# Performance work log

Measured on AMD Instinct MI355X. Metric: run time of the kernel, lower is better.

The kernel has to match this reference:

```python
import jax, jax.numpy as jnp
import numpy as np

N_NODES = 20000
N_EDGES = 80000
D = 128       # in_dim_node == in_dim_edge == hidden dims
ITERS = 15    # mp_iterations
EPS = 1e-5    # torch LayerNorm default eps


def _mlp(h, W0, b0, W1, b1, W2, b2, gamma, beta):
    """Linear-ReLU-Linear-ReLU-Linear-LayerNorm (hidden_layers=2)."""
    h = jax.nn.relu(h @ W0 + b0)
    h = jax.nn.relu(h @ W1 + b1)
    h = h @ W2 + b2
    mu = jnp.mean(h, axis=-1, keepdims=True)
    var = jnp.var(h, axis=-1, keepdims=True)
    return gamma * (h - mu) * jax.lax.rsqrt(var + EPS) + beta


def setup_inputs() -> dict:
    key = jax.random.key(0)
    ks = iter(jax.random.split(key, 32))

    def lin(fi, fo):
        bnd = 1.0 / np.sqrt(fi)
        W = jax.random.uniform(next(ks), (ITERS, fi, fo), minval=-bnd, maxval=bnd, dtype=jnp.float32)
        b = jax.random.uniform(next(ks), (ITERS, fo), minval=-bnd, maxval=bnd, dtype=jnp.float32)
        return W, b

    x = jax.random.normal(next(ks), (N_NODES, D), dtype=jnp.float32)
    edge_attr = jax.random.normal(next(ks), (N_EDGES, D), dtype=jnp.float32)
    edge_index = jax.random.randint(next(ks), (2, N_EDGES), 0, N_NODES)

    eW0, eB0 = lin(3 * D, D)   # edge MLP input = cat(src, dest, edge) = 384
    eW1, eB1 = lin(D, D)
    eW2, eB2 = lin(D, D)
    nW0, nB0 = lin(2 * D, D)   # node MLP input = cat(x, agg) = 256
    nW1, nB1 = lin(D, D)
    nW2, nB2 = lin(D, D)
    ones = jnp.ones((ITERS, D), jnp.float32)
    zeros = jnp.zeros((ITERS, D), jnp.float32)

    return dict(x=x, edge_attr=edge_attr,
                eW0=eW0, eB0=eB0, eW1=eW1, eB1=eB1, eW2=eW2, eB2=eB2, eG=ones, eBeta=zeros,
                nW0=nW0, nB0=nB0, nW1=nW1, nB1=nB1, nW2=nW2, nB2=nB2, nG=ones, nBeta=zeros,
                edge_index=edge_index)


def reference(x, edge_attr, eW0, eB0, eW1, eB1, eW2, eB2, eG, eBeta,
              nW0, nB0, nW1, nB1, nW2, nB2, nG, nBeta, edge_index):
    row, col = edge_index[0], edge_index[1]
    n = x.shape[0]
    params = (eW0, eB0, eW1, eB1, eW2, eB2, eG, eBeta,
              nW0, nB0, nW1, nB1, nW2, nB2, nG, nBeta)

    def step(carry, p):
        xc, ec = carry
        (ew0, eb0, ew1, eb1, ew2, eb2, eg, ebt,
         nw0, nb0, nw1, nb1, nw2, nb2, ng, nbt) = p
        # EdgeProcessor: gather + MLP, then FullResidualConnection (add previous)
        e_in = jnp.concatenate([xc[row], xc[col], ec], axis=-1)        # [E, 3D]
        ec = _mlp(e_in, ew0, eb0, ew1, eb1, ew2, eb2, eg, ebt) + ec
        # NodeProcessor: scatter_sum over destination nodes + MLP + residual
        agg = jax.ops.segment_sum(ec, col, num_segments=n)             # [N, D]
        n_in = jnp.concatenate([xc, agg], axis=-1)                     # [N, 2D]
        xc = _mlp(n_in, nw0, nb0, nw1, nb1, nw2, nb2, ng, nbt) + xc
        return (xc, ec), None

    (x, edge_attr), _ = jax.lax.scan(step, (x, edge_attr), params)
    return x, edge_attr
```

## Files before the change

### kernel.cpp

```cpp
#include <hip/hip_runtime.h>
#include <hip/hip_bf16.h>

typedef __hip_bfloat16 bf16;
typedef __attribute__((ext_vector_type(8))) short short8;
typedef __attribute__((ext_vector_type(4))) float f32x4;

#define NN 20000
#define NE 80000
#define DD 128
#define NITER 15
#define HSTRIDE 136

__device__ inline void gload16(const void* g, void* l) {
  __builtin_amdgcn_global_load_lds(
      (const __attribute__((address_space(1))) void*)g,
      (__attribute__((address_space(3))) void*)l, 16, 0, 0);
}

__device__ inline float bfbits2f(unsigned int hi16) {
  union { unsigned int u; float f; } c; c.u = hi16; return c.f;
}

__device__ inline float readin(const void* p, int i, int fl) {
  return fl ? (float)((const bf16*)p)[i] : ((const float*)p)[i];
}

__global__ void detzero_kernel(const unsigned short* __restrict__ x,
                               int* __restrict__ counts, int* __restrict__ flag) {
  const int bid = blockIdx.x, t = threadIdx.x;
  if (bid < 79) {
    int i = bid * 256 + t;
    if (i < NN) counts[i] = 0;
    return;
  }
  __shared__ int cs[256], ct[256];
  int sane = 0, tot = 0;
  for (int i = 2 * t; i < 16384; i += 512) {
    unsigned short v = x[i];
    int e = (v >> 7) & 0xFF;
    tot++;
    if (v == 0 || (e >= 80 && e <= 170)) sane++;
  }
  cs[t] = sane; ct[t] = tot;
  __syncthreads();
  for (int o = 128; o > 0; o >>= 1) {
    if (t < o) { cs[t] += cs[t + o]; ct[t] += ct[t + o]; }
    __syncthreads();
  }
  if (t == 0) *flag = (cs[0] * 10 > ct[0] * 7) ? 1 : 0;
}

#define CX  (NN * DD)
#define CE  (NE * DD)
#define CW0 (NITER * 384 * DD)
#define CW1 (NITER * 128 * DD)
#define CNW0 (NITER * 256 * DD)
#define CB  (NITER * DD)
#define BX0 CX
#define BX1 (BX0 + CE)
#define BX7 (BX1 + CW0 + CW1 + CW1 + CNW0 + CW1 + CW1)
#define BX8 (BX7 + 10 * CB)

struct CvtP {
  const void *x, *e;
  const void* w[6];
  bf16 *xb, *eb;
  bf16* wt[6];
  const void* bs[10];
  float* bd[10];
  const int* flag;
};

__global__ void convert_all(CvtP P) {
  const int fl = *P.flag;
  const int gstride = gridDim.x * 256;
  for (int i = blockIdx.x * 256 + threadIdx.x; i < BX8; i += gstride) {
    if (i < BX0) {
      P.xb[i] = (bf16)readin(P.x, i, fl);
    } else if (i < BX1) {
      P.eb[i - BX0] = (bf16)readin(P.e, i - BX0, fl);
    } else if (i < BX7) {
      int j = i - BX1, w;
      if (j < CW0) { w = 0; }
      else if ((j -= CW0) < CW1) { w = 1; }
      else if ((j -= CW1) < CW1) { w = 2; }
      else if ((j -= CW1) < CNW0) { w = 3; }
      else if ((j -= CNW0) < CW1) { w = 4; }
      else { j -= CW1; w = 5; }
      const int K = (w == 0) ? 384 : (w == 3) ? 256 : 128;
      float v = readin(P.w[w], j, fl);
      int it = j / (K * DD);
      int rem = j - it * K * DD;
      int k = rem >> 7, n = rem & 127;
      P.wt[w][(size_t)it * K * DD + (size_t)n * K + k] = (bf16)v;
    } else {
      int j = i - BX7;
      int b = j / CB, r = j - b * CB;
      P.bd[b][r] = readin(P.bs[b], r, fl);
    }
  }
}

template<int K0, int AMODE>
__global__ __launch_bounds__(256, 4) void fused_mlp(
    const bf16* S0b,
    const bf16* S1b,
    const int*  __restrict__ eidx,
    const bf16* __restrict__ W0t, const bf16* __restrict__ W1t,
    const bf16* __restrict__ W2t,
    const float* __restrict__ b0, const float* __restrict__ b1,
    const float* __restrict__ b2,
    const float* __restrict__ gamma, const float* __restrict__ beta,
    bf16* st, int M)
{
  constexpr int NS1 = K0 / 32;
  __shared__ __align__(16) bf16 Bls[2][128 * 32];
  __shared__ __align__(16) bf16 Hls[64 * HSTRIDE];

  const int tid  = threadIdx.x;
  const int lane = tid & 63;
  const int wv   = tid >> 6;
  const int l15  = lane & 15, quad = lane >> 4;
  const int m0   = blockIdx.x * 64;
  const int scol = tid >> 2;
  const int sk8  = (tid & 3) * 8;

  const int rowm = min(m0 + wv * 16 + l15, M - 1);
  int ir = 0, ic = 0;
  if (AMODE == 1) { ir = eidx[rowm]; ic = eidx[NE + rowm]; }

  auto dmaW = [&](const bf16* W, int K, int kk, int buf) {
    gload16(W + (size_t)scol * K + kk + sk8,        &Bls[buf][scol * 32 + sk8]);
    gload16(W + (size_t)(scol + 64) * K + kk + sk8, &Bls[buf][(scol + 64) * 32 + sk8]);
  };
  auto gatherA = [&](int kk, short8* a) {
    const int ks = (kk & 127) + quad * 8;
    const bf16* base;
    if (AMODE == 1) {
      const int seg = kk >> 7;
      base = (seg == 0) ? S0b + (size_t)ir * DD
           : (seg == 1) ? S0b + (size_t)ic * DD
                        : S1b + (size_t)rowm * DD;
    } else {
      base = (kk >> 7) ? S1b + (size_t)rowm * DD
                       : S0b + (size_t)rowm * DD;
    }
    *a = *(const short8*)(base + ks);
  };

  f32x4 acc[8];
  auto zacc = [&]() {
#pragma unroll
    for (int j = 0; j < 8; j++) acc[j] = (f32x4){0.f, 0.f, 0.f, 0.f};
  };
  auto slabMfmaA = [&](short8 a, int buf) {
    short8 bfr[8];
#pragma unroll
    for (int ni = 0; ni < 8; ni++)
      bfr[ni] = *(const short8*)&Bls[buf][(ni * 16 + l15) * 32 + quad * 8];
#pragma unroll
    for (int ni = 0; ni < 8; ni++)
      acc[ni] = __builtin_amdgcn_mfma_f32_16x16x32_bf16(a, bfr[ni], acc[ni], 0, 0, 0);
  };
  auto slabMfmaH = [&](int kk, int buf) {
    short8 a = *(const short8*)&Hls[(wv * 16 + l15) * HSTRIDE + kk + quad * 8];
    short8 bfr[8];
#pragma unroll
    for (int ni = 0; ni < 8; ni++)
      bfr[ni] = *(const short8*)&Bls[buf][(ni * 16 + l15) * 32 + quad * 8];
#pragma unroll
    for (int ni = 0; ni < 8; ni++)
      acc[ni] = __builtin_amdgcn_mfma_f32_16x16x32_bf16(a, bfr[ni], acc[ni], 0, 0, 0);
  };
  auto writeH = [&](const float* bias) {
    float bv[8];
#pragma unroll
    for (int ni = 0; ni < 8; ni++) bv[ni] = bias[ni * 16 + l15];
#pragma unroll
    for (int r = 0; r < 4; r++) {
      const int row = wv * 16 + quad * 4 + r;
#pragma unroll
      for (int ni = 0; ni < 8; ni++)
        Hls[row * HSTRIDE + ni * 16 + l15] = (bf16)fmaxf(acc[ni][r] + bv[ni], 0.f);
    }
  };

  zacc();
  short8 aCur, aNxt;
  dmaW(W0t, K0, 0, 0);
  gatherA(0, &aCur);
  __syncthreads();
#pragma unroll
  for (int s = 0; s < NS1; s++) {
    if (s + 1 < NS1) {
      dmaW(W0t, K0, (s + 1) * 32, (s + 1) & 1);
      gatherA((s + 1) * 32, &aNxt);
    } else {
      dmaW(W1t, 128, 0, NS1 & 1);
    }
    slabMfmaA(aCur, s & 1);
    __syncthreads();
    aCur = aNxt;
  }
  writeH(b0);
  __syncthreads();

  zacc();
#pragma unroll
  for (int s = 0; s < 4; s++) {
    if (s < 3) dmaW(W1t, 128, (s + 1) * 32, (NS1 + s + 1) & 1);
    else       dmaW(W2t, 128, 0,            (NS1 + 4) & 1);
    slabMfmaH(s * 32, (NS1 + s) & 1);
    __syncthreads();
  }
  writeH(b1);
  __syncthreads();

  zacc();
#pragma unroll
  for (int s = 0; s < 4; s++) {
    if (s < 3) dmaW(W2t, 128, (s + 1) * 32, (NS1 + 4 + s + 1) & 1);
    slabMfmaH(s * 32, (NS1 + 4 + s) & 1);
    if (s < 3) __syncthreads();
  }

  float bv[8], gv[8], btv[8];
#pragma unroll
  for (int ni = 0; ni < 8; ni++) {
    const int col = ni * 16 + l15;
    bv[ni] = b2[col]; gv[ni] = gamma[col]; btv[ni] = beta[col];
  }
#pragma unroll
  for (int r = 0; r < 4; r++) {
    float a = 0.f, bq = 0.f;
#pragma unroll
    for (int ni = 0; ni < 8; ni++) {
      const float v = acc[ni][r] + bv[ni];
      a += v; bq += v * v;
    }
#pragma unroll
    for (int off = 1; off < 16; off <<= 1) {
      a  += __shfl_xor(a, off);
      bq += __shfl_xor(bq, off);
    }
    const float mu = a * (1.0f / 128.0f);
    const float var = fmaxf(bq * (1.0f / 128.0f) - mu * mu, 0.0f);
    const float rs = rsqrtf(var + 1e-5f);
    const int m = m0 + wv * 16 + quad * 4 + r;
    if (m < M) {
#pragma unroll
      for (int ni = 0; ni < 8; ni++) {
        const int col = ni * 16 + l15;
        const float v = acc[ni][r] + bv[ni];
        const float lnv = (v - mu) * rs * gv[ni] + btv[ni];
        const size_t idx = (size_t)m * DD + col;
        st[idx] = (bf16)(lnv + (float)st[idx]);
      }
    }
  }
}

__global__ void hist_kernel(const int* __restrict__ eidx, int* __restrict__ counts) {
  int e = blockIdx.x * 256 + threadIdx.x;
  if (e < NE) atomicAdd(&counts[eidx[NE + e]], 1);
}

__global__ void scan_kernel(const int* __restrict__ counts, int* __restrict__ offs,
                            int* __restrict__ cursor) {
  __shared__ int sums[1024];
  const int t = threadIdx.x;
  const int base = t * 20;
  int local[20];
  int s = 0;
  for (int i = 0; i < 20; i++) {
    int idx = base + i;
    int c = (idx < NN) ? counts[idx] : 0;
    local[i] = s; s += c;
  }
  sums[t] = s;
  __syncthreads();
  for (int off = 1; off < 1024; off <<= 1) {
    int v = 0;
    if (t >= off) v = sums[t - off];
    __syncthreads();
    if (t >= off) sums[t] += v;
    __syncthreads();
  }
  int excl = (t == 0) ? 0 : sums[t - 1];
  for (int i = 0; i < 20; i++) {
    int idx = base + i;
    if (idx < NN) { offs[idx] = excl + local[i]; cursor[idx] = 0; }
  }
  if (t == 1023) offs[NN] = sums[1023];
}

__global__ void fill_kernel(const int* __restrict__ eidx, const int* __restrict__ offs,
                            int* __restrict__ cursor, int* __restrict__ sorted) {
  int e = blockIdx.x * 256 + threadIdx.x;
  if (e < NE) {
    int n = eidx[NE + e];
    int p = atomicAdd(&cursor[n], 1);
    sorted[offs[n] + p] = e;
  }
}

__global__ void aggregate_kernel(const bf16* __restrict__ eb, const int* __restrict__ offs,
                                 const int* __restrict__ sorted, bf16* __restrict__ aggb) {
  const int node = blockIdx.x * 4 + (threadIdx.x >> 6);
  const int lane = threadIdx.x & 63;
  if (node >= NN) return;
  const int s = offs[node], t = offs[node + 1];
  float a0 = 0.f, a1 = 0.f;
  for (int i = s; i < t; i++) {
    const int e = sorted[i];
    unsigned int v = *(const unsigned int*)(eb + (size_t)e * DD + 2 * lane);
    a0 += bfbits2f(v << 16);
    a1 += bfbits2f(v & 0xFFFF0000u);
  }
  bf16 o0 = (bf16)a0, o1 = (bf16)a1;
  unsigned int pack = (unsigned int)(*(unsigned short*)&o0)
                    | ((unsigned int)(*(unsigned short*)&o1) << 16);
  *(unsigned int*)(aggb + (size_t)node * DD + 2 * lane) = pack;
}

__global__ void outwb_kernel(const bf16* __restrict__ xb, const bf16* __restrict__ eb,
                             void* __restrict__ out, const int* __restrict__ flag) {
  int i = blockIdx.x * 256 + threadIdx.x;
  const int nx = NN * DD, total = (NN + NE) * DD;
  if (i < total) {
    bf16 v = (i < nx) ? xb[i] : eb[i - nx];
    if (*flag) ((bf16*)out)[i] = v;
    else       ((float*)out)[i] = (float)v;
  }
}

extern "C" void kernel_launch(void* const* d_in, const int* in_sizes, int n_in,
                              void* d_out, int out_size, void* d_ws, size_t ws_size,
                              hipStream_t stream) {
  const int* eidx = (const int*)d_in[18];

  char* ws = (char*)d_ws;
  size_t off = 0;
  auto alloc = [&](size_t bytes) -> char* {
    char* p = ws + off;
    off = (off + bytes + 255) & ~(size_t)255;
    return p;
  };

  bf16* xb   = (bf16*)alloc((size_t)NN * DD * 2);
  bf16* eb   = (bf16*)alloc((size_t)NE * DD * 2);
  bf16* aggb = (bf16*)alloc((size_t)NN * DD * 2);
  bf16* eW0t = (bf16*)alloc((size_t)CW0 * 2);
  bf16* eW1t = (bf16*)alloc((size_t)CW1 * 2);
  bf16* eW2t = (bf16*)alloc((size_t)CW1 * 2);
  bf16* nW0t = (bf16*)alloc((size_t)CNW0 * 2);
  bf16* nW1t = (bf16*)alloc((size_t)CW1 * 2);
  bf16* nW2t = (bf16*)alloc((size_t)CW1 * 2);
  float* bf_[10];
  for (int i = 0; i < 10; i++) bf_[i] = (float*)alloc(CB * 4);
  int* counts = (int*)alloc((size_t)NN * 4);
  int* cursor = (int*)alloc((size_t)NN * 4);
  int* offs   = (int*)alloc((size_t)(NN + 1) * 4);
  int* sorted = (int*)alloc((size_t)NE * 4);
  int* flag   = (int*)alloc(4);

  detzero_kernel<<<80, 256, 0, stream>>>((const unsigned short*)d_in[0], counts, flag);

  CvtP C;
  C.x = d_in[0]; C.e = d_in[1];
  C.w[0] = d_in[2];  C.w[1] = d_in[4];  C.w[2] = d_in[6];
  C.w[3] = d_in[10]; C.w[4] = d_in[12]; C.w[5] = d_in[14];
  C.xb = xb; C.eb = eb;
  C.wt[0] = eW0t; C.wt[1] = eW1t; C.wt[2] = eW2t;
  C.wt[3] = nW0t; C.wt[4] = nW1t; C.wt[5] = nW2t;
  const int bsrc_idx[10] = {3, 5, 7, 8, 9, 11, 13, 15, 16, 17};
  for (int i = 0; i < 10; i++) { C.bs[i] = d_in[bsrc_idx[i]]; C.bd[i] = bf_[i]; }
  C.flag = flag;
  convert_all<<<2048, 256, 0, stream>>>(C);

  hist_kernel<<<(NE + 255) / 256, 256, 0, stream>>>(eidx, counts);
  scan_kernel<<<1, 1024, 0, stream>>>(counts, offs, cursor);
  fill_kernel<<<(NE + 255) / 256, 256, 0, stream>>>(eidx, offs, cursor, sorted);

  const int egrid = NE / 64;
  const int ngrid = (NN + 63) / 64;

  for (int t = 0; t < NITER; t++) {
    fused_mlp<384, 1><<<egrid, 256, 0, stream>>>(
        xb, eb, eidx,
        eW0t + (size_t)t * 384 * DD, eW1t + (size_t)t * 128 * DD,
        eW2t + (size_t)t * 128 * DD,
        bf_[0] + t * DD, bf_[1] + t * DD, bf_[2] + t * DD,
        bf_[3] + t * DD, bf_[4] + t * DD, eb, NE);
    aggregate_kernel<<<(NN + 3) / 4, 256, 0, stream>>>(eb, offs, sorted, aggb);
    fused_mlp<256, 2><<<ngrid, 256, 0, stream>>>(
        xb, aggb, nullptr,
        nW0t + (size_t)t * 256 * DD, nW1t + (size_t)t * 128 * DD,
        nW2t + (size_t)t * 128 * DD,
        bf_[5] + t * DD, bf_[6] + t * DD, bf_[7] + t * DD,
        bf_[8] + t * DD, bf_[9] + t * DD, xb, NN);
  }

  outwb_kernel<<<((NN + NE) * DD + 255) / 256, 256, 0, stream>>>(xb, eb, d_out, flag);
}
```

Baseline: 1.142 ms.

## Load MLP weights directly from global into registers, two M-tiles per wave for edges

Drops the double-buffered LDS staging of weight slabs, which relied on global_load_lds DMA plus block barriers. Each lane now reads its B fragments straight from global memory (L2-resident weights) into registers. A template parameter MI lets a wave process 32 rows instead of 16, so each B fragment is reused across two MFMA row groups. The edge MLP uses MI=2 with half as many blocks and lower occupancy bounds. This removes the syncthreads and LDS traffic for weights but makes every wave issue its own global weight loads, and register pressure rises.

```diff
diff --git a/kernel.cpp b/kernel.cpp
--- a/kernel.cpp
+++ b/kernel.cpp
@@ -10,12 +10,6 @@
 #define DD 128
 #define NITER 15
 #define HSTRIDE 136
-
-__device__ inline void gload16(const void* g, void* l) {
-  __builtin_amdgcn_global_load_lds(
-      (const __attribute__((address_space(1))) void*)g,
-      (__attribute__((address_space(3))) void*)l, 16, 0, 0);
-}
 
 __device__ inline float bfbits2f(unsigned int hi16) {
   union { unsigned int u; float f; } c; c.u = hi16; return c.f;
@@ -101,8 +95,8 @@
   }
 }
 
-template<int K0, int AMODE>
-__global__ __launch_bounds__(256, 4) void fused_mlp(
+template<int K0, int AMODE, int MI>
+__global__ __launch_bounds__(256, MI == 1 ? 4 : 2) void fused_mlp(
     const bf16* S0b,
     const bf16* S1b,
     const int*  __restrict__ eidx,
@@ -113,115 +107,118 @@
     const float* __restrict__ gamma, const float* __restrict__ beta,
     bf16* st, int M)
 {
-  constexpr int NS1 = K0 / 32;
-  __shared__ __align__(16) bf16 Bls[2][128 * 32];
-  __shared__ __align__(16) bf16 Hls[64 * HSTRIDE];
+  constexpr int RPW = 16 * MI;
+  __shared__ __align__(16) bf16 Hls[64 * MI * HSTRIDE];
 
   const int tid  = threadIdx.x;
   const int lane = tid & 63;
   const int wv   = tid >> 6;
   const int l15  = lane & 15, quad = lane >> 4;
-  const int m0   = blockIdx.x * 64;
-  const int scol = tid >> 2;
-  const int sk8  = (tid & 3) * 8;
-
-  const int rowm = min(m0 + wv * 16 + l15, M - 1);
-  int ir = 0, ic = 0;
-  if (AMODE == 1) { ir = eidx[rowm]; ic = eidx[NE + rowm]; }
-
-  auto dmaW = [&](const bf16* W, int K, int kk, int buf) {
-    gload16(W + (size_t)scol * K + kk + sk8,        &Bls[buf][scol * 32 + sk8]);
-    gload16(W + (size_t)(scol + 64) * K + kk + sk8, &Bls[buf][(scol + 64) * 32 + sk8]);
+  const int m0   = blockIdx.x * (64 * MI);
+
+  int rowm[MI], ir[MI], ic[MI];
+#pragma unroll
+  for (int g = 0; g < MI; g++) {
+    rowm[g] = min(m0 + wv * RPW + g * 16 + l15, M - 1);
+    if (AMODE == 1) { ir[g] = eidx[rowm[g]]; ic[g] = eidx[NE + rowm[g]]; }
+  }
+
+  const bf16* pB[8];
+  auto setB = [&](const bf16* __restrict__ W, int K) {
+#pragma unroll
+    for (int ni = 0; ni < 8; ni++)
+      pB[ni] = W + (size_t)(ni * 16 + l15) * K + quad * 8;
   };
-  auto gatherA = [&](int kk, short8* a) {
+
+  f32x4 acc[MI][8];
+  auto zacc = [&]() {
+#pragma unroll
+    for (int g = 0; g < MI; g++)
+#pragma unroll
+      for (int ni = 0; ni < 8; ni++) acc[g][ni] = (f32x4){0.f, 0.f, 0.f, 0.f};
+  };
+
+  auto gatherA = [&](int g, int kk) -> short8 {
     const int ks = (kk & 127) + quad * 8;
     const bf16* base;
     if (AMODE == 1) {
       const int seg = kk >> 7;
-      base = (seg == 0) ? S0b + (size_t)ir * DD
-           : (seg == 1) ? S0b + (size_t)ic * DD
-                        : S1b + (size_t)rowm * DD;
+      base = (seg == 0) ? S0b + (size_t)ir[g] * DD
+           : (seg == 1) ? S0b + (size_t)ic[g] * DD
+                        : S1b + (size_t)rowm[g] * DD;
     } else {
-      base = (kk >> 7) ? S1b + (size_t)rowm * DD
-                       : S0b + (size_t)rowm * DD;
-    }
-    *a = *(const short8*)(base + ks);
+      base = (kk >> 7) ? S1b + (size_t)rowm[g] * DD
+                       : S0b + (size_t)rowm[g] * DD;
+    }
+    return *(const short8*)(base + ks);
   };
 
-  f32x4 acc[8];
-  auto zacc = [&]() {
-#pragma unroll
-    for (int j = 0; j < 8; j++) acc[j] = (f32x4){0.f, 0.f, 0.f, 0.f};
+  auto writeH = [&](const float* __restrict__ bias) {
+    float bv[8];
+#pragma unroll
+    for (int ni = 0; ni < 8; ni++) bv[ni] = bias[ni * 16 + l15];
+#pragma unroll
+    for (int g = 0; g < MI; g++)
+#pragma unroll
+      for (int r = 0; r < 4; r++) {
+        const int row = wv * RPW + g * 16 + quad * 4 + r;
+#pragma unroll
+        for (int ni = 0; ni < 8; ni++)
+          Hls[row * HSTRIDE + ni * 16 + l15] = (bf16)fmaxf(acc[g][ni][r] + bv[ni], 0.f);
+      }
   };
-  auto slabMfmaA = [&](short8 a, int buf) {
+
+  zacc();
+  setB(W0t, K0);
+#pragma unroll
+  for (int s = 0; s < K0 / 32; s++) {
+    const int kk = s * 32;
     short8 bfr[8];
 #pragma unroll
-    for (int ni = 0; ni < 8; ni++)
-      bfr[ni] = *(const short8*)&Bls[buf][(ni * 16 + l15) * 32 + quad * 8];
-#pragma unroll
-    for (int ni = 0; ni < 8; ni++)
-      acc[ni] = __builtin_amdgcn_mfma_f32_16x16x32_bf16(a, bfr[ni], acc[ni], 0, 0, 0);
-  };
-  auto slabMfmaH = [&](int kk, int buf) {
-    short8 a = *(const short8*)&Hls[(wv * 16 + l15) * HSTRIDE + kk + quad * 8];
+    for (int ni = 0; ni < 8; ni++) bfr[ni] = *(const short8*)(pB[ni] + kk);
+#pragma unroll
+    for (int g = 0; g < MI; g++) {
+      short8 a = gatherA(g, kk);
+#pragma unroll
+      for (int ni = 0; ni < 8; ni++)
+        acc[g][ni] = __builtin_amdgcn_mfma_f32_16x16x32_bf16(a, bfr[ni], acc[g][ni], 0, 0, 0);
+    }
+  }
+  writeH(b0);
+
+  zacc();
+  setB(W1t, 128);
+#pragma unroll
+  for (int s = 0; s < 4; s++) {
+    const int kk = s * 32;
     short8 bfr[8];
 #pragma unroll
-    for (int ni = 0; ni < 8; ni++)
-      bfr[ni] = *(const short8*)&Bls[buf][(ni * 16 + l15) * 32 + quad * 8];
-#pragma unroll
-    for (int ni = 0; ni < 8; ni++)
-      acc[ni] = __builtin_amdgcn_mfma_f32_16x16x32_bf16(a, bfr[ni], acc[ni], 0, 0, 0);
-  };
-  auto writeH = [&](const float* bias) {
-    float bv[8];
-#pragma unroll
-    for (int ni = 0; ni < 8; ni++) bv[ni] = bias[ni * 16 + l15];
-#pragma unroll
-    for (int r = 0; r < 4; r++) {
-      const int row = wv * 16 + quad * 4 + r;
+    for (int ni = 0; ni < 8; ni++) bfr[ni] = *(const short8*)(pB[ni] + kk);
+#pragma unroll
+    for (int g = 0; g < MI; g++) {
+      short8 a = *(const short8*)&Hls[(wv * RPW + g * 16 + l15) * HSTRIDE + kk + quad * 8];
 #pragma unroll
       for (int ni = 0; ni < 8; ni++)
-        Hls[row * HSTRIDE + ni * 16 + l15] = (bf16)fmaxf(acc[ni][r] + bv[ni], 0.f);
-    }
-  };
+        acc[g][ni] = __builtin_amdgcn_mfma_f32_16x16x32_bf16(a, bfr[ni], acc[g][ni], 0, 0, 0);
+    }
+  }
+  writeH(b1);
 
   zacc();
-  short8 aCur, aNxt;
-  dmaW(W0t, K0, 0, 0);
-  gatherA(0, &aCur);
-  __syncthreads();
-#pragma unroll
-  for (int s = 0; s < NS1; s++) {
-    if (s + 1 < NS1) {
-      dmaW(W0t, K0, (s + 1) * 32, (s + 1) & 1);
-      gatherA((s + 1) * 32, &aNxt);
-    } else {
-      dmaW(W1t, 128, 0, NS1 & 1);
-    }
-    slabMfmaA(aCur, s & 1);
-    __syncthreads();
-    aCur = aNxt;
-  }
-  writeH(b0);
-  __syncthreads();
-
-  zacc();
+  setB(W2t, 128);
 #pragma unroll
   for (int s = 0; s < 4; s++) {
-    if (s < 3) dmaW(W1t, 128, (s + 1) * 32, (NS1 + s + 1) & 1);
-    else       dmaW(W2t, 128, 0,            (NS1 + 4) & 1);
-    slabMfmaH(s * 32, (NS1 + s) & 1);
-    __syncthreads();
-  }
-  writeH(b1);
-  __syncthreads();
-
-  zacc();
-#pragma unroll
-  for (int s = 0; s < 4; s++) {
-    if (s < 3) dmaW(W2t, 128, (s + 1) * 32, (NS1 + 4 + s + 1) & 1);
-    slabMfmaH(s * 32, (NS1 + 4 + s) & 1);
-    if (s < 3) __syncthreads();
+    const int kk = s * 32;
+    short8 bfr[8];
+#pragma unroll
+    for (int ni = 0; ni < 8; ni++) bfr[ni] = *(const short8*)(pB[ni] + kk);
+#pragma unroll
+    for (int g = 0; g < MI; g++) {
+      short8 a = *(const short8*)&Hls[(wv * RPW + g * 16 + l15) * HSTRIDE + kk + quad * 8];
+#pragma unroll
+      for (int ni = 0; ni < 8; ni++)
+        acc[g][ni] = __builtin_amdgcn_mfma_f32_16x16x32_bf16(a, bfr[ni], acc[g][ni], 0, 0, 0);
+    }
   }
 
   float bv[8], gv[8], btv[8];
@@ -231,30 +228,33 @@
     bv[ni] = b2[col]; gv[ni] = gamma[col]; btv[ni] = beta[col];
   }
 #pragma unroll
-  for (int r = 0; r < 4; r++) {
-    float a = 0.f, bq = 0.f;
-#pragma unroll
-    for (int ni = 0; ni < 8; ni++) {
-      const float v = acc[ni][r] + bv[ni];
-      a += v; bq += v * v;
-    }
-#pragma unroll
-    for (int off = 1; off < 16; off <<= 1) {
-      a  += __shfl_xor(a, off);
-      bq += __shfl_xor(bq, off);
-    }
-    const float mu = a * (1.0f / 128.0f);
-    const float var = fmaxf(bq * (1.0f / 128.0f) - mu * mu, 0.0f);
-    const float rs = rsqrtf(var + 1e-5f);
-    const int m = m0 + wv * 16 + quad * 4 + r;
-    if (m < M) {
+  for (int g = 0; g < MI; g++) {
+#pragma unroll
+    for (int r = 0; r < 4; r++) {
+      float a = 0.f, bq = 0.f;
 #pragma unroll
       for (int ni = 0; ni < 8; ni++) {
-        const int col = ni * 16 + l15;
-        const float v = acc[ni][r] + bv[ni];
-        const float lnv = (v - mu) * rs * gv[ni] + btv[ni];
-        const size_t idx = (size_t)m * DD + col;
-        st[idx] = (bf16)(lnv + (float)st[idx]);
+        const float v = acc[g][ni][r] + bv[ni];
+        a += v; bq += v * v;
+      }
+#pragma unroll
+      for (int off = 1; off < 16; off <<= 1) {
+        a  += __shfl_xor(a, off);
+        bq += __shfl_xor(bq, off);
+      }
+      const float mu = a * (1.0f / 128.0f);
+      const float var = fmaxf(bq * (1.0f / 128.0f) - mu * mu, 0.0f);
+      const float rs = rsqrtf(var + 1e-5f);
+      const int m = m0 + wv * RPW + g * 16 + quad * 4 + r;
+      if (m < M) {
+#pragma unroll
+        for (int ni = 0; ni < 8; ni++) {
+          const int col = ni * 16 + l15;
+          const float v = acc[g][ni][r] + bv[ni];
+          const float lnv = (v - mu) * rs * gv[ni] + btv[ni];
+          const size_t idx = (size_t)m * DD + col;
+          st[idx] = (bf16)(lnv + (float)st[idx]);
+        }
       }
     }
   }
@@ -382,18 +382,18 @@
   scan_kernel<<<1, 1024, 0, stream>>>(counts, offs, cursor);
   fill_kernel<<<(NE + 255) / 256, 256, 0, stream>>>(eidx, offs, cursor, sorted);
 
-  const int egrid = NE / 64;
+  const int egrid = NE / 128;
   const int ngrid = (NN + 63) / 64;
 
   for (int t = 0; t < NITER; t++) {
-    fused_mlp<384, 1><<<egrid, 256, 0, stream>>>(
+    fused_mlp<384, 1, 2><<<egrid, 256, 0, stream>>>(
         xb, eb, eidx,
         eW0t + (size_t)t * 384 * DD, eW1t + (size_t)t * 128 * DD,
         eW2t + (size_t)t * 128 * DD,
         bf_[0] + t * DD, bf_[1] + t * DD, bf_[2] + t * DD,
         bf_[3] + t * DD, bf_[4] + t * DD, eb, NE);
     aggregate_kernel<<<(NN + 3) / 4, 256, 0, stream>>>(eb, offs, sorted, aggb);
-    fused_mlp<256, 2><<<ngrid, 256, 0, stream>>>(
+    fused_mlp<256, 2, 1><<<ngrid, 256, 0, stream>>>(
         xb, aggb, nullptr,
         nW0t + (size_t)t * 256 * DD, nW1t + (size_t)t * 128 * DD,
         nW2t + (size_t)t * 128 * DD,
```

After: 2.029 ms. 1.78x slower.

## Fuse segment-sum aggregation into node MLP and read weights directly from global

Applied to the files above, without the earlier changes.

Removes the separate aggregate kernel and the aggb buffer: the node MLP now gathers each tile's 64 destination-node sums through the CSR offsets and writes them into a new LDS tile that feeds the first GEMM. It also drops the LDS double-buffered global_load_lds staging of weight slabs and the __syncthreads around it, so each lane loads B fragments straight from global memory. The intent is to save one launch per iteration plus the aggregate round trip through HBM, and to cut barrier overhead. The risks are that the aggregation runs serially (16 nodes per wave) inside only ~313 node blocks, so parallelism is low, and that weight fragments are re-read from global/L2 by every wave instead of being shared through LDS.

```diff
diff --git a/kernel.cpp b/kernel.cpp
--- a/kernel.cpp
+++ b/kernel.cpp
@@ -10,12 +10,6 @@
 #define DD 128
 #define NITER 15
 #define HSTRIDE 136
-
-__device__ inline void gload16(const void* g, void* l) {
-  __builtin_amdgcn_global_load_lds(
-      (const __attribute__((address_space(1))) void*)g,
-      (__attribute__((address_space(3))) void*)l, 16, 0, 0);
-}
 
 __device__ inline float bfbits2f(unsigned int hi16) {
   union { unsigned int u; float f; } c; c.u = hi16; return c.f;
@@ -106,6 +100,8 @@
     const bf16* S0b,
     const bf16* S1b,
     const int*  __restrict__ eidx,
+    const int*  __restrict__ offs,
+    const int*  __restrict__ sorted,
     const bf16* __restrict__ W0t, const bf16* __restrict__ W1t,
     const bf16* __restrict__ W2t,
     const float* __restrict__ b0, const float* __restrict__ b1,
@@ -113,115 +109,119 @@
     const float* __restrict__ gamma, const float* __restrict__ beta,
     bf16* st, int M)
 {
-  constexpr int NS1 = K0 / 32;
-  __shared__ __align__(16) bf16 Bls[2][128 * 32];
   __shared__ __align__(16) bf16 Hls[64 * HSTRIDE];
+  __shared__ __align__(16) bf16 Als[(AMODE == 2) ? 64 * HSTRIDE : 16];
 
   const int tid  = threadIdx.x;
   const int lane = tid & 63;
   const int wv   = tid >> 6;
   const int l15  = lane & 15, quad = lane >> 4;
   const int m0   = blockIdx.x * 64;
-  const int scol = tid >> 2;
-  const int sk8  = (tid & 3) * 8;
 
   const int rowm = min(m0 + wv * 16 + l15, M - 1);
   int ir = 0, ic = 0;
   if (AMODE == 1) { ir = eidx[rowm]; ic = eidx[NE + rowm]; }
 
-  auto dmaW = [&](const bf16* W, int K, int kk, int buf) {
-    gload16(W + (size_t)scol * K + kk + sk8,        &Bls[buf][scol * 32 + sk8]);
-    gload16(W + (size_t)(scol + 64) * K + kk + sk8, &Bls[buf][(scol + 64) * 32 + sk8]);
-  };
-  auto gatherA = [&](int kk, short8* a) {
+  if (AMODE == 2) {
+    for (int g = 0; g < 16; ++g) {
+      const int node = min(m0 + wv * 16 + g, M - 1);
+      const int s = offs[node], t = offs[node + 1];
+      float a0 = 0.f, a1 = 0.f;
+      for (int i = s; i < t; i++) {
+        const int e = sorted[i];
+        unsigned int v = *(const unsigned int*)(S1b + (size_t)e * DD + 2 * lane);
+        a0 += bfbits2f(v << 16);
+        a1 += bfbits2f(v & 0xFFFF0000u);
+      }
+      bf16 o0 = (bf16)a0, o1 = (bf16)a1;
+      unsigned int pack = (unsigned int)(*(unsigned short*)&o0)
+                        | ((unsigned int)(*(unsigned short*)&o1) << 16);
+      *(unsigned int*)&Als[(wv * 16 + g) * HSTRIDE + 2 * lane] = pack;
+    }
+  }
+
+  const bf16* pB[8];
+  auto setB = [&](const bf16* __restrict__ W, int K) {
+#pragma unroll
+    for (int ni = 0; ni < 8; ni++)
+      pB[ni] = W + (size_t)(ni * 16 + l15) * K + quad * 8;
+  };
+
+  f32x4 acc[8];
+  auto zacc = [&]() {
+#pragma unroll
+    for (int ni = 0; ni < 8; ni++) acc[ni] = (f32x4){0.f, 0.f, 0.f, 0.f};
+  };
+
+  auto gatherA = [&](int kk) -> short8 {
     const int ks = (kk & 127) + quad * 8;
-    const bf16* base;
     if (AMODE == 1) {
       const int seg = kk >> 7;
-      base = (seg == 0) ? S0b + (size_t)ir * DD
-           : (seg == 1) ? S0b + (size_t)ic * DD
-                        : S1b + (size_t)rowm * DD;
+      const bf16* base = (seg == 0) ? S0b + (size_t)ir * DD
+                       : (seg == 1) ? S0b + (size_t)ic * DD
+                                    : S1b + (size_t)rowm * DD;
+      return *(const short8*)(base + ks);
     } else {
-      base = (kk >> 7) ? S1b + (size_t)rowm * DD
-                       : S0b + (size_t)rowm * DD;
-    }
-    *a = *(const short8*)(base + ks);
-  };
-
-  f32x4 acc[8];
-  auto zacc = [&]() {
-#pragma unroll
-    for (int j = 0; j < 8; j++) acc[j] = (f32x4){0.f, 0.f, 0.f, 0.f};
-  };
-  auto slabMfmaA = [&](short8 a, int buf) {
+      if (kk >> 7) return *(const short8*)&Als[(wv * 16 + l15) * HSTRIDE + ks];
+      return *(const short8*)(S0b + (size_t)rowm * DD + ks);
+    }
+  };
+
+  auto writeH = [&](const float* __restrict__ bias) {
+    float bv[8];
+#pragma unroll
+    for (int ni = 0; ni < 8; ni++) bv[ni] = bias[ni * 16 + l15];
+#pragma unroll
+    for (int r = 0; r < 4; r++) {
+      const int row = wv * 16 + quad * 4 + r;
+#pragma unroll
+      for (int ni = 0; ni < 8; ni++)
+        Hls[row * HSTRIDE + ni * 16 + l15] = (bf16)fmaxf(acc[ni][r] + bv[ni], 0.f);
+    }
+  };
+
+  zacc();
+  setB(W0t, K0);
+#pragma unroll
+  for (int s = 0; s < K0 / 32; s++) {
+    const int kk = s * 32;
     short8 bfr[8];
 #pragma unroll
-    for (int ni = 0; ni < 8; ni++)
-      bfr[ni] = *(const short8*)&Bls[buf][(ni * 16 + l15) * 32 + quad * 8];
+    for (int ni = 0; ni < 8; ni++) bfr[ni] = *(const short8*)(pB[ni] + kk);
+    short8 a = gatherA(kk);
 #pragma unroll
     for (int ni = 0; ni < 8; ni++)
       acc[ni] = __builtin_amdgcn_mfma_f32_16x16x32_bf16(a, bfr[ni], acc[ni], 0, 0, 0);
-  };
-  auto slabMfmaH = [&](int kk, int buf) {
+  }
+  writeH(b0);
+
+  zacc();
+  setB(W1t, 128);
+#pragma unroll
+  for (int s = 0; s < 4; s++) {
+    const int kk = s * 32;
+    short8 bfr[8];
+#pragma unroll
+    for (int ni = 0; ni < 8; ni++) bfr[ni] = *(const short8*)(pB[ni] + kk);
     short8 a = *(const short8*)&Hls[(wv * 16 + l15) * HSTRIDE + kk + quad * 8];
-    short8 bfr[8];
-#pragma unroll
-    for (int ni = 0; ni < 8; ni++)
-      bfr[ni] = *(const short8*)&Bls[buf][(ni * 16 + l15) * 32 + quad * 8];
 #pragma unroll
     for (int ni = 0; ni < 8; ni++)
       acc[ni] = __builtin_amdgcn_mfma_f32_16x16x32_bf16(a, bfr[ni], acc[ni], 0, 0, 0);
-  };
-  auto writeH = [&](const float* bias) {
-    float bv[8];
-#pragma unroll
-    for (int ni = 0; ni < 8; ni++) bv[ni] = bias[ni * 16 + l15];
-#pragma unroll
-    for (int r = 0; r < 4; r++) {
-      const int row = wv * 16 + quad * 4 + r;
-#pragma unroll
-      for (int ni = 0; ni < 8; ni++)
-        Hls[row * HSTRIDE + ni * 16 + l15] = (bf16)fmaxf(acc[ni][r] + bv[ni], 0.f);
-    }
-  };
+  }
+  writeH(b1);
 
   zacc();
-  short8 aCur, aNxt;
-  dmaW(W0t, K0, 0, 0);
-  gatherA(0, &aCur);
-  __syncthreads();
-#pragma unroll
-  for (int s = 0; s < NS1; s++) {
-    if (s + 1 < NS1) {
-      dmaW(W0t, K0, (s + 1) * 32, (s + 1) & 1);
-      gatherA((s + 1) * 32, &aNxt);
-    } else {
-      dmaW(W1t, 128, 0, NS1 & 1);
-    }
-    slabMfmaA(aCur, s & 1);
-    __syncthreads();
-    aCur = aNxt;
-  }
-  writeH(b0);
-  __syncthreads();
-
-  zacc();
+  setB(W2t, 128);
 #pragma unroll
   for (int s = 0; s < 4; s++) {
-    if (s < 3) dmaW(W1t, 128, (s + 1) * 32, (NS1 + s + 1) & 1);
-    else       dmaW(W2t, 128, 0,            (NS1 + 4) & 1);
-    slabMfmaH(s * 32, (NS1 + s) & 1);
-    __syncthreads();
-  }
-  writeH(b1);
-  __syncthreads();
-
-  zacc();
-#pragma unroll
-  for (int s = 0; s < 4; s++) {
-    if (s < 3) dmaW(W2t, 128, (s + 1) * 32, (NS1 + 4 + s + 1) & 1);
-    slabMfmaH(s * 32, (NS1 + 4 + s) & 1);
-    if (s < 3) __syncthreads();
+    const int kk = s * 32;
+    short8 bfr[8];
+#pragma unroll
+    for (int ni = 0; ni < 8; ni++) bfr[ni] = *(const short8*)(pB[ni] + kk);
+    short8 a = *(const short8*)&Hls[(wv * 16 + l15) * HSTRIDE + kk + quad * 8];
+#pragma unroll
+    for (int ni = 0; ni < 8; ni++)
+      acc[ni] = __builtin_amdgcn_mfma_f32_16x16x32_bf16(a, bfr[ni], acc[ni], 0, 0, 0);
   }
 
   float bv[8], gv[8], btv[8];
@@ -304,25 +304,6 @@
   }
 }
 
-__global__ void aggregate_kernel(const bf16* __restrict__ eb, const int* __restrict__ offs,
-                                 const int* __restrict__ sorted, bf16* __restrict__ aggb) {
-  const int node = blockIdx.x * 4 + (threadIdx.x >> 6);
-  const int lane = threadIdx.x & 63;
-  if (node >= NN) return;
-  const int s = offs[node], t = offs[node + 1];
-  float a0 = 0.f, a1 = 0.f;
-  for (int i = s; i < t; i++) {
-    const int e = sorted[i];
-    unsigned int v = *(const unsigned int*)(eb + (size_t)e * DD + 2 * lane);
-    a0 += bfbits2f(v << 16);
-    a1 += bfbits2f(v & 0xFFFF0000u);
-  }
-  bf16 o0 = (bf16)a0, o1 = (bf16)a1;
-  unsigned int pack = (unsigned int)(*(unsigned short*)&o0)
-                    | ((unsigned int)(*(unsigned short*)&o1) << 16);
-  *(unsigned int*)(aggb + (size_t)node * DD + 2 * lane) = pack;
-}
-
 __global__ void outwb_kernel(const bf16* __restrict__ xb, const bf16* __restrict__ eb,
                              void* __restrict__ out, const int* __restrict__ flag) {
   int i = blockIdx.x * 256 + threadIdx.x;
@@ -349,7 +330,6 @@
 
   bf16* xb   = (bf16*)alloc((size_t)NN * DD * 2);
   bf16* eb   = (bf16*)alloc((size_t)NE * DD * 2);
-  bf16* aggb = (bf16*)alloc((size_t)NN * DD * 2);
   bf16* eW0t = (bf16*)alloc((size_t)CW0 * 2);
   bf16* eW1t = (bf16*)alloc((size_t)CW1 * 2);
   bf16* eW2t = (bf16*)alloc((size_t)CW1 * 2);
@@ -387,14 +367,13 @@
 
   for (int t = 0; t < NITER; t++) {
     fused_mlp<384, 1><<<egrid, 256, 0, stream>>>(
-        xb, eb, eidx,
+        xb, eb, eidx, nullptr, nullptr,
         eW0t + (size_t)t * 384 * DD, eW1t + (size_t)t * 128 * DD,
         eW2t + (size_t)t * 128 * DD,
         bf_[0] + t * DD, bf_[1] + t * DD, bf_[2] + t * DD,
         bf_[3] + t * DD, bf_[4] + t * DD, eb, NE);
-    aggregate_kernel<<<(NN + 3) / 4, 256, 0, stream>>>(eb, offs, sorted, aggb);
     fused_mlp<256, 2><<<ngrid, 256, 0, stream>>>(
-        xb, aggb, nullptr,
+        xb, eb, nullptr, offs, sorted,
         nW0t + (size_t)t * 256 * DD, nW1t + (size_t)t * 128 * DD,
         nW2t + (size_t)t * 128 * DD,
         bf_[5] + t * DD, bf_[6] + t * DD, bf_[7] + t * DD,
```

After: 2.961 ms. 2.59x slower.
